# Kernel optimization log

Measured on AMD Instinct MI355X. Metric: run time of the kernel, lower is better.

The kernel has to match this reference:

```python
import jax, jax.numpy as jnp
import numpy as np

B, H, W, C = 8, 64, 64, 256
NUM_GROUPS = 32
EPS = 1e-6  # flax GroupNorm default


def setup_inputs() -> dict:
    key = jax.random.key(0)
    ks = jax.random.split(key, 9)
    x = jax.random.normal(ks[0], (B, H, W, C), dtype=jnp.float32)
    init = lambda k, shape: jax.random.normal(k, shape, dtype=jnp.float32) * 0.02
    return {
        "x": x,
        "gn_scale": jnp.ones((C,), jnp.float32),
        "gn_bias": jnp.zeros((C,), jnp.float32),
        "wq": init(ks[1], (C, C)), "bq": jnp.zeros((C,), jnp.float32),
        "wk": init(ks[2], (C, C)), "bk": jnp.zeros((C,), jnp.float32),
        "wv": init(ks[3], (C, C)), "bv": jnp.zeros((C,), jnp.float32),
        "wo": init(ks[4], (C, C)), "bo": jnp.zeros((C,), jnp.float32),
    }


def group_norm(x, scale, bias, num_groups, eps):
    b, h, w, c = x.shape
    xg = x.reshape(b, h, w, num_groups, c // num_groups)
    mean = jnp.mean(xg, axis=(1, 2, 4), keepdims=True)
    var = jnp.mean(jnp.square(xg - mean), axis=(1, 2, 4), keepdims=True)
    xn = (xg - mean) * jax.lax.rsqrt(var + eps)
    return xn.reshape(b, h, w, c) * scale + bias


def reference(x, gn_scale, gn_bias, wq, bq, wk, bk, wv, bv, wo, bo):
    b, h, w, c = x.shape
    hn = group_norm(x, gn_scale, gn_bias, NUM_GROUPS, EPS)
    hf = hn.reshape(b, h * w, c)  # (B, S, C)
    q = hf @ wq + bq
    k = hf @ wk + bk
    v = hf @ wv + bv
    scaling = jnp.sqrt(jnp.float32(c)).astype(x.dtype)
    attn = jax.nn.softmax(jnp.einsum('bsc,btc->bst', q, k) / scaling, axis=-1)
    out = jnp.einsum('bst,btc->bsc', attn, v)
    out = out @ wo + bo
    return out.reshape(b, h, w, c) + x
```

## Files before the change

kernel.cpp:

```cpp
#include <hip/hip_runtime.h>

#define NB   8
#define SS   4096
#define CC   256
#define NG   32
#define CPG  8
#define EPSV 1e-6f
#define MTOT (NB * SS)

typedef short bf16x8 __attribute__((ext_vector_type(8)));
typedef unsigned short u16x8 __attribute__((ext_vector_type(8)));
typedef float f32x4  __attribute__((ext_vector_type(4)));
typedef float f32x16 __attribute__((ext_vector_type(16)));
typedef int   i32x4  __attribute__((ext_vector_type(4)));
typedef int   i32x8  __attribute__((ext_vector_type(8)));
typedef unsigned char u8;

typedef __attribute__((address_space(1))) const unsigned int as1_u32;
typedef __attribute__((address_space(3))) unsigned int as3_u32;

__device__ __forceinline__ unsigned short f2bf(float f) {
  unsigned int u = __builtin_bit_cast(unsigned int, f);
  u = (u + 0x7FFFu + ((u >> 16) & 1u)) >> 16;
  return (unsigned short)u;
}
__device__ __forceinline__ u8 f2fp8(float f) {
  return (u8)(__builtin_amdgcn_cvt_pk_fp8_f32(f, f, 0, 0) & 0xFF);
}
__device__ __forceinline__ void dma16(const u8* src, u8* lds) {
  __builtin_amdgcn_global_load_lds((as1_u32*)src, (as3_u32*)lds, 16, 0, 0);
}
__device__ __forceinline__ float fast_exp2(float x) {
#if __has_builtin(__builtin_amdgcn_exp2f)
  return __builtin_amdgcn_exp2f(x);
#else
  return exp2f(x);
#endif
}

__global__ __launch_bounds__(256) void gn_stats_part_kernel(
    const float* __restrict__ x, float* __restrict__ part) {
  const int b = blockIdx.x >> 5, slice = blockIdx.x & 31;
  const int tid = threadIdx.x;
  const int g = tid & 31;
  const int p8 = tid >> 5;
  const float* base = x + ((size_t)(b * SS + slice * 128 + p8) * CC + g * CPG);
  float s = 0.f, ss = 0.f;
#pragma unroll
  for (int it = 0; it < 16; it++) {
    const float4* p = (const float4*)(base + (size_t)it * 8 * CC);
    float4 a = p[0], c = p[1];
    s  += (a.x + a.y) + (a.z + a.w) + (c.x + c.y) + (c.z + c.w);
    ss += (a.x*a.x + a.y*a.y) + (a.z*a.z + a.w*a.w)
        + (c.x*c.x + c.y*c.y) + (c.z*c.z + c.w*c.w);
  }
  s  += __shfl_xor(s, 32);
  ss += __shfl_xor(ss, 32);
  __shared__ float lsum[4][32], lssum[4][32];
  const int wv = tid >> 6, lane = tid & 63;
  if (lane < 32) { lsum[wv][lane] = s; lssum[wv][lane] = ss; }
  __syncthreads();
  if (tid < 32) {
    float ts  = (lsum[0][tid] + lsum[1][tid]) + (lsum[2][tid] + lsum[3][tid]);
    float tss = (lssum[0][tid] + lssum[1][tid]) + (lssum[2][tid] + lssum[3][tid]);
    float* dst = part + ((size_t)(b * 32 + tid) * 32 + slice) * 2;
    dst[0] = ts; dst[1] = tss;
  }
}

__global__ __launch_bounds__(256) void prep_wt_kernel(
    const float* __restrict__ w0, const float* __restrict__ w1,
    const float* __restrict__ w2, const float* __restrict__ w3,
    unsigned short* __restrict__ wt,
    const float* __restrict__ part, float* __restrict__ stats) {
  __shared__ float t[64][68];
  if (blockIdx.y == 4) {
    if (blockIdx.x == 0) {
      const int bg = threadIdx.x;
      const float* src = part + (size_t)bg * 64;
      float s = 0.f, ss = 0.f;
#pragma unroll
      for (int sl = 0; sl < 32; sl++) { s += src[sl * 2]; ss += src[sl * 2 + 1]; }
      const float inv = 1.f / (float)(SS * CPG);
      float mean = s * inv;
      float var  = ss * inv - mean * mean;
      stats[bg * 2]     = mean;
      stats[bg * 2 + 1] = rsqrtf(var + EPSV);
    }
    return;
  }
  int which = blockIdx.y;
  const float* W = (which == 0) ? w0 : (which == 1) ? w1 : (which == 2) ? w2 : w3;
  int tx = (blockIdx.x & 3) * 64;
  int ty = (blockIdx.x >> 2) * 64;
  int tid = threadIdx.x;
  int row = tid >> 4;
  int col = (tid & 15) * 4;
#pragma unroll
  for (int i = 0; i < 4; i++) {
    float4 v = *(const float4*)(W + (size_t)(ty + row + i * 16) * CC + tx + col);
    *(float4*)(&t[row + i * 16][col]) = v;
  }
  __syncthreads();
#pragma unroll
  for (int i = 0; i < 4; i++) {
    int n = row + i * 16;
    ushort4 o;
    o.x = f2bf(t[col + 0][n]);
    o.y = f2bf(t[col + 1][n]);
    o.z = f2bf(t[col + 2][n]);
    o.w = f2bf(t[col + 3][n]);
    *(ushort4*)(wt + (size_t)which * CC * CC + (size_t)(tx + n) * CC + ty + col) = o;
  }
}

__global__ __launch_bounds__(256) void gn_norm_kernel(const float* __restrict__ x,
                                                      const float* __restrict__ stats,
                                                      const float* __restrict__ gamma,
                                                      const float* __restrict__ beta,
                                                      unsigned short* __restrict__ hn) {
  int i8 = blockIdx.x * 256 + threadIdx.x;
  int c8 = (i8 & 31) * 8;
  size_t row = (size_t)(i8 >> 5);
  int b = (int)(row >> 12);
  int sidx = (b * NG + (c8 >> 3)) * 2;
  float mean = stats[sidx], rstd = stats[sidx + 1];
  const float4* xp = (const float4*)(x + row * CC + c8);
  float4 v0 = xp[0], v1 = xp[1];
  const float4* gp = (const float4*)(gamma + c8);
  float4 g0 = gp[0], g1 = gp[1];
  const float4* bp = (const float4*)(beta + c8);
  float4 b0 = bp[0], b1 = bp[1];
  u16x8 o;
  o[0] = f2bf((v0.x - mean) * rstd * g0.x + b0.x);
  o[1] = f2bf((v0.y - mean) * rstd * g0.y + b0.y);
  o[2] = f2bf((v0.z - mean) * rstd * g0.z + b0.z);
  o[3] = f2bf((v0.w - mean) * rstd * g0.w + b0.w);
  o[4] = f2bf((v1.x - mean) * rstd * g1.x + b1.x);
  o[5] = f2bf((v1.y - mean) * rstd * g1.y + b1.y);
  o[6] = f2bf((v1.z - mean) * rstd * g1.z + b1.z);
  o[7] = f2bf((v1.w - mean) * rstd * g1.w + b1.w);
  *(u16x8*)(hn + row * CC + c8) = o;
}


__global__ __launch_bounds__(256) void qkv_gemm_kernel(
    const unsigned short* __restrict__ A,
    const unsigned short* __restrict__ WT,
    const float* __restrict__ bq, const float* __restrict__ bk, const float* __restrict__ bv,
    u8* __restrict__ qo, u8* __restrict__ ko, u8* __restrict__ vt) {
  __shared__ __align__(1024) u8 smem[65536];
  u8* As0 = smem;
  u8* As1 = smem + 16384;
  u8* Bs  = smem + 32768;

  const int which = blockIdx.z;
  const u8* Bwb = (const u8*)(WT + (size_t)which * CC * CC);
  const float* bias = (which == 0) ? bq : (which == 1) ? bk : bv;

  const int m0 = blockIdx.x * 256;
  const int n0 = blockIdx.y * 64;
  const int tid = threadIdx.x;
  const int wave = tid >> 6, lane = tid & 63;
  const int l32 = lane & 31, h = lane >> 5;

  const u8* Ab = (const u8*)A;

  const int am = tid >> 2;
  const int aslot = tid & 3;
  const size_t asrc_row = (size_t)(m0 + am) * 512;
  const int asrc_ch = ((aslot ^ (am & 3)) << 4);
  const int bn = tid >> 5;
  const int bslot = tid & 31;

#pragma unroll
  for (int i = 0; i < 8; i++) {
    int n = i * 8 + bn;
    dma16(Bwb + (size_t)(n0 + n) * 512 + ((bslot ^ (n & 31)) << 4),
          Bs + i * 4096 + tid * 16);
  }
#pragma unroll
  for (int i = 0; i < 4; i++)
    dma16(Ab + asrc_row + (size_t)i * 64 * 512 + asrc_ch, As0 + i * 4096 + tid * 16);
  __syncthreads();

  f32x16 acc[2][2] = {};
  const int arow0 = (wave * 64 + l32) * 64;
  const int nrow0 = l32 * 512;
  const int aswz = l32 & 3;
  const int bswz = l32;

#pragma unroll
  for (int s = 0; s < 8; ++s) {
    u8* cur = (s & 1) ? As1 : As0;
    if (s < 7) {
      u8* nxt = (s & 1) ? As0 : As1;
      size_t koff = (size_t)(s + 1) * 64;
#pragma unroll
      for (int i = 0; i < 4; i++)
        dma16(Ab + asrc_row + (size_t)i * 64 * 512 + koff + asrc_ch,
              nxt + i * 4096 + tid * 16);
    }
#pragma unroll
    for (int ks = 0; ks < 2; ks++) {
      bf16x8 af0 = *(const bf16x8*)(cur + arow0 + (((h + 2 * ks) ^ aswz) << 4));
      bf16x8 af1 = *(const bf16x8*)(cur + arow0 + 32 * 64 + (((h + 2 * ks) ^ aswz) << 4));
      bf16x8 bf0 = *(const bf16x8*)(Bs + nrow0 + (((s * 4 + h + 2 * ks) ^ bswz) << 4));
      bf16x8 bf1 = *(const bf16x8*)(Bs + nrow0 + 32 * 512 + (((s * 4 + h + 2 * ks) ^ bswz) << 4));
      acc[0][0] = __builtin_amdgcn_mfma_f32_32x32x16_bf16(af0, bf0, acc[0][0], 0, 0, 0);
      acc[0][1] = __builtin_amdgcn_mfma_f32_32x32x16_bf16(af0, bf1, acc[0][1], 0, 0, 0);
      acc[1][0] = __builtin_amdgcn_mfma_f32_32x32x16_bf16(af1, bf0, acc[1][0], 0, 0, 0);
      acc[1][1] = __builtin_amdgcn_mfma_f32_32x32x16_bf16(af1, bf1, acc[1][1], 0, 0, 0);
    }
    __syncthreads();
  }

  if (which < 2) {
    u8* out = (which == 0) ? qo : ko;
#pragma unroll
    for (int nt = 0; nt < 2; nt++) {
      int n = n0 + nt * 32 + l32;
      float bv_ = bias[n];
#pragma unroll
      for (int mt = 0; mt < 2; mt++)
#pragma unroll
        for (int r = 0; r < 16; r++) {
          int m = m0 + wave * 64 + mt * 32 + (r & 3) + 8 * (r >> 2) + 4 * h;
          out[(size_t)m * CC + n] = f2fp8(acc[mt][nt][r] + bv_);
        }
    }
  } else {
    int bb = m0 >> 12;
#pragma unroll
    for (int nt = 0; nt < 2; nt++) {
      int n = n0 + nt * 32 + l32;
      float bv_ = bias[n];
#pragma unroll
      for (int mt = 0; mt < 2; mt++)
#pragma unroll
        for (int g = 0; g < 4; g++) {
          int mg = m0 + wave * 64 + mt * 32 + g * 8 + 4 * h;
          int w = __builtin_amdgcn_cvt_pk_fp8_f32(acc[mt][nt][g*4+0] + bv_, acc[mt][nt][g*4+1] + bv_, 0, 0);
          w = __builtin_amdgcn_cvt_pk_fp8_f32(acc[mt][nt][g*4+2] + bv_, acc[mt][nt][g*4+3] + bv_, w, 1);
          *(unsigned int*)(vt + (size_t)bb * CC * SS + (size_t)n * SS + (mg & 4095)) = (unsigned int)w;
        }
    }
  }
}

__global__ __launch_bounds__(256) void out_gemm_kernel(
    const unsigned short* __restrict__ A,
    const unsigned short* __restrict__ WT,
    const float* __restrict__ bias,
    const float* __restrict__ residual,
    float* __restrict__ Of) {
  __shared__ __align__(1024) u8 smem[65536];
  u8* As0 = smem;
  u8* As1 = smem + 16384;
  u8* Bs  = smem + 32768;

  const u8* Bwb = (const u8*)(WT + (size_t)3 * CC * CC);
  const int m0 = blockIdx.x * 256;
  const int n0 = blockIdx.y * 64;
  const int tid = threadIdx.x;
  const int wave = tid >> 6, lane = tid & 63;
  const int l32 = lane & 31, h = lane >> 5;

  const u8* Ab = (const u8*)A;
  const int am = tid >> 2;
  const int aslot = tid & 3;
  const size_t asrc_row = (size_t)(m0 + am) * 512;
  const int asrc_ch = ((aslot ^ (am & 3)) << 4);
  const int bn = tid >> 5;
  const int bslot = tid & 31;

#pragma unroll
  for (int i = 0; i < 8; i++) {
    int n = i * 8 + bn;
    dma16(Bwb + (size_t)(n0 + n) * 512 + ((bslot ^ (n & 31)) << 4),
          Bs + i * 4096 + tid * 16);
  }
#pragma unroll
  for (int i = 0; i < 4; i++)
    dma16(Ab + asrc_row + (size_t)i * 64 * 512 + asrc_ch, As0 + i * 4096 + tid * 16);
  __syncthreads();

  f32x16 acc[2][2] = {};
  const int arow0 = (wave * 64 + l32) * 64;
  const int nrow0 = l32 * 512;
  const int aswz = l32 & 3;
  const int bswz = l32;

#pragma unroll
  for (int s = 0; s < 8; ++s) {
    u8* cur = (s & 1) ? As1 : As0;
    if (s < 7) {
      u8* nxt = (s & 1) ? As0 : As1;
      size_t koff = (size_t)(s + 1) * 64;
#pragma unroll
      for (int i = 0; i < 4; i++)
        dma16(Ab + asrc_row + (size_t)i * 64 * 512 + koff + asrc_ch,
              nxt + i * 4096 + tid * 16);
    }
#pragma unroll
    for (int ks = 0; ks < 2; ks++) {
      bf16x8 af0 = *(const bf16x8*)(cur + arow0 + (((h + 2 * ks) ^ aswz) << 4));
      bf16x8 af1 = *(const bf16x8*)(cur + arow0 + 32 * 64 + (((h + 2 * ks) ^ aswz) << 4));
      bf16x8 bf0 = *(const bf16x8*)(Bs + nrow0 + (((s * 4 + h + 2 * ks) ^ bswz) << 4));
      bf16x8 bf1 = *(const bf16x8*)(Bs + nrow0 + 32 * 512 + (((s * 4 + h + 2 * ks) ^ bswz) << 4));
      acc[0][0] = __builtin_amdgcn_mfma_f32_32x32x16_bf16(af0, bf0, acc[0][0], 0, 0, 0);
      acc[0][1] = __builtin_amdgcn_mfma_f32_32x32x16_bf16(af0, bf1, acc[0][1], 0, 0, 0);
      acc[1][0] = __builtin_amdgcn_mfma_f32_32x32x16_bf16(af1, bf0, acc[1][0], 0, 0, 0);
      acc[1][1] = __builtin_amdgcn_mfma_f32_32x32x16_bf16(af1, bf1, acc[1][1], 0, 0, 0);
    }
    __syncthreads();
  }

#pragma unroll
  for (int nt = 0; nt < 2; nt++) {
    int n = n0 + nt * 32 + l32;
    float bv_ = bias[n];
#pragma unroll
    for (int mt = 0; mt < 2; mt++)
#pragma unroll
      for (int r = 0; r < 16; r++) {
        int m = m0 + wave * 64 + mt * 32 + (r & 3) + 8 * (r >> 2) + 4 * h;
        Of[(size_t)m * CC + n] = acc[mt][nt][r] + bv_ + residual[(size_t)m * CC + n];
      }
  }
}

#define BR 64

__global__ __launch_bounds__(256, 2) void flash_attn_kernel(
    const u8* __restrict__ Qg,
    const u8* __restrict__ Kg,
    const u8* __restrict__ Vtg,
    unsigned short* __restrict__ Og) {
  __shared__ __align__(1024) u8 smem[65536 + 512];
  u8* KA  = smem;
  u8* KBb = smem + 16384;
  u8* VB  = smem + 32768;

  const int bid = blockIdx.x;
  const int b = bid & 7, q0 = (bid >> 3) * BR;
  const int tid = threadIdx.x;
  const int wave = tid >> 6, lane = tid & 63;
  const int l32 = lane & 31, h = lane >> 5;
  const int wm = wave >> 1, wn = wave & 1;

  const u8* Qb  = Qg  + (size_t)b * SS * CC;
  const u8* Kb  = Kg  + (size_t)b * SS * CC;
  const u8* Vtb = Vtg + (size_t)b * CC * SS;

  const int kkey = tid >> 4, kc16 = tid & 15;
  const u8* ksrc0 = Kb + (size_t)kkey * CC + ((kc16 ^ (kkey & 15)) << 4);
  const int vch = tid >> 3;
  const int vs  = (tid & 7) ^ (vch & 7);
  const u8* vsrc0 = Vtb + (size_t)vch * SS + (vs << 4);

  i32x8 qf[4];
  {
    const u8* qrow = Qb + (size_t)(q0 + wm * 32 + l32) * CC + h * 32;
#pragma unroll
    for (int t = 0; t < 4; t++) qf[t] = *(const i32x8*)(qrow + t * 64);
  }

  f32x16 oacc[8] = {};
  float ll = 0.f;

#pragma unroll
  for (int i = 0; i < 4; i++)
    dma16(ksrc0 + (size_t)i * 16 * CC, KA + i * 4096 + tid * 16);

  const int kswz = l32 & 15;
  const int vswz = l32 & 7;

  for (int jp = 0; jp < 32; ++jp) {
    int w0[4], w1[4], o0[4];

    __syncthreads();
    {
      size_t krow = (size_t)jp * 128 + 64;
#pragma unroll
      for (int i = 0; i < 4; i++)
        dma16(ksrc0 + (krow + (size_t)i * 16) * CC, KBb + i * 4096 + tid * 16);
      size_t vbase = (size_t)jp * 128;
#pragma unroll
      for (int i = 0; i < 8; i++)
        dma16(vsrc0 + (size_t)i * 32 * SS + vbase, VB + i * 4096 + tid * 16);
    }
    {
      f32x16 sacc = {};
      const u8* kb = KA + (wn * 32 + l32) * 256;
      __builtin_amdgcn_s_setprio(1);
#pragma unroll
      for (int t = 0; t < 4; t++) {
        i32x4 r0 = *(const i32x4*)(kb + (((t * 4 + 2 * h)     ^ kswz) << 4));
        i32x4 r1 = *(const i32x4*)(kb + (((t * 4 + 2 * h + 1) ^ kswz) << 4));
        i32x8 kf = __builtin_shufflevector(r0, r1, 0, 1, 2, 3, 4, 5, 6, 7);
        sacc = __builtin_amdgcn_mfma_scale_f32_32x32x64_f8f6f4(
            kf, qf[t], sacc, 0, 0, 0, 0x7F7F7F7F, 0, 0x7F7F7F7F);
      }
      __builtin_amdgcn_s_setprio(0);
#pragma unroll
      for (int g = 0; g < 4; g++) {
        float p0 = fast_exp2(fminf(sacc[g * 4 + 0] * 0.09016844f, 7.213475f));
        float p1 = fast_exp2(fminf(sacc[g * 4 + 1] * 0.09016844f, 7.213475f));
        float p2 = fast_exp2(fminf(sacc[g * 4 + 2] * 0.09016844f, 7.213475f));
        float p3 = fast_exp2(fminf(sacc[g * 4 + 3] * 0.09016844f, 7.213475f));
        ll += (p0 + p1) + (p2 + p3);
        int wv_ = __builtin_amdgcn_cvt_pk_fp8_f32(p0, p1, 0, 0);
        w0[g] = __builtin_amdgcn_cvt_pk_fp8_f32(p2, p3, wv_, 1);
      }
#pragma unroll
      for (int g = 0; g < 4; g++) o0[g] = __shfl_xor(w0[g], 32);
    }

    __syncthreads();
    if (jp + 1 < 32) {
      size_t krow = (size_t)(jp + 1) * 128;
#pragma unroll
      for (int i = 0; i < 4; i++)
        dma16(ksrc0 + (krow + (size_t)i * 16) * CC, KA + i * 4096 + tid * 16);
    }
    {
      f32x16 sacc = {};
      const u8* kb = KBb + (wn * 32 + l32) * 256;
      __builtin_amdgcn_s_setprio(1);
#pragma unroll
      for (int t = 0; t < 4; t++) {
        i32x4 r0 = *(const i32x4*)(kb + (((t * 4 + 2 * h)     ^ kswz) << 4));
        i32x4 r1 = *(const i32x4*)(kb + (((t * 4 + 2 * h + 1) ^ kswz) << 4));
        i32x8 kf = __builtin_shufflevector(r0, r1, 0, 1, 2, 3, 4, 5, 6, 7);
        sacc = __builtin_amdgcn_mfma_scale_f32_32x32x64_f8f6f4(
            kf, qf[t], sacc, 0, 0, 0, 0x7F7F7F7F, 0, 0x7F7F7F7F);
      }
      __builtin_amdgcn_s_setprio(0);
#pragma unroll
      for (int g = 0; g < 4; g++) {
        float p0 = fast_exp2(fminf(sacc[g * 4 + 0] * 0.09016844f, 7.213475f));
        float p1 = fast_exp2(fminf(sacc[g * 4 + 1] * 0.09016844f, 7.213475f));
        float p2 = fast_exp2(fminf(sacc[g * 4 + 2] * 0.09016844f, 7.213475f));
        float p3 = fast_exp2(fminf(sacc[g * 4 + 3] * 0.09016844f, 7.213475f));
        ll += (p0 + p1) + (p2 + p3);
        int wv_ = __builtin_amdgcn_cvt_pk_fp8_f32(p0, p1, 0, 0);
        w1[g] = __builtin_amdgcn_cvt_pk_fp8_f32(p2, p3, wv_, 1);
      }
    }

    int pa_[8];
#pragma unroll
    for (int g = 0; g < 4; g++) {
      int o1 = __shfl_xor(w1[g], 32);
      pa_[2 * g]     = (h == 0) ? w0[g] : o1;
      pa_[2 * g + 1] = (h == 0) ? o0[g] : w1[g];
    }
    i32x8 pa = {pa_[0], pa_[1], pa_[2], pa_[3], pa_[4], pa_[5], pa_[6], pa_[7]};

    __builtin_amdgcn_s_setprio(1);
#pragma unroll
    for (int nt = 0; nt < 8; nt++) {
      const u8* vb = VB + (nt * 32 + l32) * 128;
      i32x4 r0 = *(const i32x4*)(vb + (((4 * h + 2 * wn)     ^ vswz) << 4));
      i32x4 r1 = *(const i32x4*)(vb + (((4 * h + 2 * wn + 1) ^ vswz) << 4));
      i32x8 vf = __builtin_shufflevector(r0, r1, 0, 1, 2, 3, 4, 5, 6, 7);
      oacc[nt] = __builtin_amdgcn_mfma_scale_f32_32x32x64_f8f6f4(
          pa, vf, oacc[nt], 0, 0, 0, 0x7F7F7F7F, 0, 0x7F7F7F7F);
    }
    __builtin_amdgcn_s_setprio(0);
  }

  __syncthreads();
  ll += __shfl_xor(ll, 32);
  float* Lred = (float*)(smem + 65536);
  if (h == 0) Lred[wn * 64 + wm * 32 + l32] = ll;

  float* scratch = (float*)smem;
  {
    float* z = scratch + (size_t)(wm * 2 + (1 - wn)) * 4096;
#pragma unroll
    for (int ntg = 0; ntg < 8; ntg++) {
      if ((ntg >> 2) != wn) {
        int nt = ntg & 3;
#pragma unroll
        for (int r = 0; r < 16; r++) {
          int row = (r & 3) + 8 * (r >> 2) + 4 * h;
          z[row * 128 + nt * 32 + l32] = oacc[ntg][r];
        }
      }
    }
  }
  __syncthreads();
  {
    const float* z = scratch + (size_t)(wm * 2 + wn) * 4096;
#pragma unroll
    for (int ntg = 0; ntg < 8; ntg++) {
      if ((ntg >> 2) == wn) {
        int nt = ntg & 3;
#pragma unroll
        for (int r = 0; r < 16; r++) {
          int row = (r & 3) + 8 * (r >> 2) + 4 * h;
          float inv = 1.f / (Lred[wm * 32 + row] + Lred[64 + wm * 32 + row]);
          float v = oacc[ntg][r] + z[row * 128 + nt * 32 + l32];
          Og[((size_t)b * SS + q0 + wm * 32 + row) * CC + wn * 128 + nt * 32 + l32]
              = f2bf(v * inv);
        }
      }
    }
  }
}

extern "C" void kernel_launch(void* const* d_in, const int* in_sizes, int n_in,
                              void* d_out, int out_size, void* d_ws, size_t ws_size,
                              hipStream_t stream) {
  const float* x   = (const float*)d_in[0];
  const float* gsc = (const float*)d_in[1];
  const float* gbi = (const float*)d_in[2];
  const float* wq  = (const float*)d_in[3];
  const float* bq  = (const float*)d_in[4];
  const float* wk  = (const float*)d_in[5];
  const float* bk  = (const float*)d_in[6];
  const float* wv  = (const float*)d_in[7];
  const float* bv  = (const float*)d_in[8];
  const float* wo  = (const float*)d_in[9];
  const float* bo  = (const float*)d_in[10];
  float* out = (float*)d_out;

  char* ws = (char*)d_ws;
  const size_t MAT = (size_t)MTOT * CC;
  float* stats        = (float*)ws;
  unsigned short* wt  = (unsigned short*)(ws + 4096);
  unsigned short* hn  = wt + (size_t)4 * CC * CC;
  unsigned short* ao  = hn + MAT;
  u8* q  = (u8*)(ao + MAT);
  u8* k  = q + MAT;
  u8* vt = k + MAT;

  float* part = (float*)ao;

  gn_stats_part_kernel<<<NB * NG, 256, 0, stream>>>(x, part);
  prep_wt_kernel<<<dim3(16, 5), 256, 0, stream>>>(wq, wk, wv, wo, wt, part, stats);
  gn_norm_kernel<<<(int)(MAT / 8 / 256), 256, 0, stream>>>(x, stats, gsc, gbi, hn);

  qkv_gemm_kernel<<<dim3(MTOT / 256, CC / 64, 3), 256, 0, stream>>>(
      hn, wt, bq, bk, bv, q, k, vt);

  flash_attn_kernel<<<NB * (SS / BR), 256, 0, stream>>>(q, k, vt, ao);

  out_gemm_kernel<<<dim3(MTOT / 256, CC / 64), 256, 0, stream>>>(ao, wt, bo, x, out);
}
```

Baseline: 244.4 us.

## Split PV output columns across waves via LDS-shared P tile for higher occupancy

Restructures the flash attention loop to process 64 keys per iteration, with each wave pair splitting the 256 output columns instead of splitting keys. P fragments are exchanged through a small swizzled LDS buffer rather than cross-lane shuffles. This halves the output accumulators and removes the final cross-wave reduction through LDS, allowing 3 blocks per CU with a smaller shared memory footprint. The trade-off is twice as many loop iterations and barriers, plus extra LDS traffic for the P tile.

```diff
diff --git a/kernel.cpp b/kernel.cpp
--- a/kernel.cpp
+++ b/kernel.cpp
@@ -332,22 +332,24 @@
 
 #define BR 64
 
-__global__ __launch_bounds__(256, 2) void flash_attn_kernel(
+__global__ __launch_bounds__(256, 3) void flash_attn_kernel(
     const u8* __restrict__ Qg,
     const u8* __restrict__ Kg,
     const u8* __restrict__ Vtg,
     unsigned short* __restrict__ Og) {
-  __shared__ __align__(1024) u8 smem[65536 + 512];
-  u8* KA  = smem;
-  u8* KBb = smem + 16384;
+  __shared__ __align__(1024) u8 smem[53760];
+  u8* KB0 = smem;
+  u8* KB1 = smem + 16384;
   u8* VB  = smem + 32768;
+  u8* Ps  = smem + 49152;
+  float* Lred = (float*)(smem + 53248);
 
   const int bid = blockIdx.x;
   const int b = bid & 7, q0 = (bid >> 3) * BR;
   const int tid = threadIdx.x;
   const int wave = tid >> 6, lane = tid & 63;
   const int l32 = lane & 31, h = lane >> 5;
-  const int wm = wave >> 1, wn = wave & 1;
+  const int wm = wave >> 1, wc = wave & 1;
 
   const u8* Qb  = Qg  + (size_t)b * SS * CC;
   const u8* Kb  = Kg  + (size_t)b * SS * CC;
@@ -355,8 +357,8 @@
 
   const int kkey = tid >> 4, kc16 = tid & 15;
   const u8* ksrc0 = Kb + (size_t)kkey * CC + ((kc16 ^ (kkey & 15)) << 4);
-  const int vch = tid >> 3;
-  const int vs  = (tid & 7) ^ (vch & 7);
+  const int vch = tid >> 2;
+  const int vs  = (tid & 3) ^ (vch & 3);
   const u8* vsrc0 = Vtb + (size_t)vch * SS + (vs << 4);
 
   i32x8 qf[4];
@@ -366,33 +368,32 @@
     for (int t = 0; t < 4; t++) qf[t] = *(const i32x8*)(qrow + t * 64);
   }
 
-  f32x16 oacc[8] = {};
+  f32x16 oacc[4] = {};
   float ll = 0.f;
 
 #pragma unroll
   for (int i = 0; i < 4; i++)
-    dma16(ksrc0 + (size_t)i * 16 * CC, KA + i * 4096 + tid * 16);
+    dma16(ksrc0 + (size_t)i * 16 * CC, KB0 + i * 4096 + tid * 16);
 
   const int kswz = l32 & 15;
-  const int vswz = l32 & 7;
-
-  for (int jp = 0; jp < 32; ++jp) {
-    int w0[4], w1[4], o0[4];
+  const int vswz = l32 & 3;
+  const int pswz = l32 & 7;
+
+  for (int j = 0; j < SS / BR; ++j) {
+    const u8* Kcur = (j & 1) ? KB1 : KB0;
+    u8* Knxt = (j & 1) ? KB0 : KB1;
 
     __syncthreads();
     {
-      size_t krow = (size_t)jp * 128 + 64;
+      size_t vbase = (size_t)j * 64;
 #pragma unroll
       for (int i = 0; i < 4; i++)
-        dma16(ksrc0 + (krow + (size_t)i * 16) * CC, KBb + i * 4096 + tid * 16);
-      size_t vbase = (size_t)jp * 128;
-#pragma unroll
-      for (int i = 0; i < 8; i++)
-        dma16(vsrc0 + (size_t)i * 32 * SS + vbase, VB + i * 4096 + tid * 16);
-    }
+        dma16(vsrc0 + (size_t)i * 64 * SS + vbase, VB + i * 4096 + tid * 16);
+    }
+
     {
       f32x16 sacc = {};
-      const u8* kb = KA + (wn * 32 + l32) * 256;
+      const u8* kb = Kcur + (wc * 32 + l32) * 256;
       __builtin_amdgcn_s_setprio(1);
 #pragma unroll
       for (int t = 0; t < 4; t++) {
@@ -403,6 +404,7 @@
             kf, qf[t], sacc, 0, 0, 0, 0x7F7F7F7F, 0, 0x7F7F7F7F);
       }
       __builtin_amdgcn_s_setprio(0);
+      u8* pb = Ps + (wm * 32 + l32) * 64;
 #pragma unroll
       for (int g = 0; g < 4; g++) {
         float p0 = fast_exp2(fminf(sacc[g * 4 + 0] * 0.09016844f, 7.213475f));
@@ -411,103 +413,57 @@
         float p3 = fast_exp2(fminf(sacc[g * 4 + 3] * 0.09016844f, 7.213475f));
         ll += (p0 + p1) + (p2 + p3);
         int wv_ = __builtin_amdgcn_cvt_pk_fp8_f32(p0, p1, 0, 0);
-        w0[g] = __builtin_amdgcn_cvt_pk_fp8_f32(p2, p3, wv_, 1);
+        wv_ = __builtin_amdgcn_cvt_pk_fp8_f32(p2, p3, wv_, 1);
+        *(unsigned int*)(pb + (((wc * 4 + g) ^ pswz) << 3) + 4 * h) = (unsigned int)wv_;
       }
-#pragma unroll
-      for (int g = 0; g < 4; g++) o0[g] = __shfl_xor(w0[g], 32);
     }
 
     __syncthreads();
-    if (jp + 1 < 32) {
-      size_t krow = (size_t)(jp + 1) * 128;
+    if (j + 1 < SS / BR) {
+      size_t krow = (size_t)(j + 1) * 64;
 #pragma unroll
       for (int i = 0; i < 4; i++)
-        dma16(ksrc0 + (krow + (size_t)i * 16) * CC, KA + i * 4096 + tid * 16);
-    }
+        dma16(ksrc0 + (krow + (size_t)i * 16) * CC, Knxt + i * 4096 + tid * 16);
+    }
+
     {
-      f32x16 sacc = {};
-      const u8* kb = KBb + (wn * 32 + l32) * 256;
+      unsigned long pf[4];
+      const u8* pb = Ps + (wm * 32 + l32) * 64;
+#pragma unroll
+      for (int ki = 0; ki < 4; ki++)
+        pf[ki] = *(const unsigned long*)(pb + (((4 * h + ki) ^ pswz) << 3));
+      i32x8 pa;
+#pragma unroll
+      for (int ki = 0; ki < 4; ki++) {
+        pa[2 * ki]     = (int)(unsigned int)pf[ki];
+        pa[2 * ki + 1] = (int)(unsigned int)(pf[ki] >> 32);
+      }
       __builtin_amdgcn_s_setprio(1);
 #pragma unroll
-      for (int t = 0; t < 4; t++) {
-        i32x4 r0 = *(const i32x4*)(kb + (((t * 4 + 2 * h)     ^ kswz) << 4));
-        i32x4 r1 = *(const i32x4*)(kb + (((t * 4 + 2 * h + 1) ^ kswz) << 4));
-        i32x8 kf = __builtin_shufflevector(r0, r1, 0, 1, 2, 3, 4, 5, 6, 7);
-        sacc = __builtin_amdgcn_mfma_scale_f32_32x32x64_f8f6f4(
-            kf, qf[t], sacc, 0, 0, 0, 0x7F7F7F7F, 0, 0x7F7F7F7F);
+      for (int nt = 0; nt < 4; nt++) {
+        const u8* vb = VB + (wc * 128 + nt * 32 + l32) * 64;
+        i32x4 r0 = *(const i32x4*)(vb + (((2 * h)     ^ vswz) << 4));
+        i32x4 r1 = *(const i32x4*)(vb + (((2 * h + 1) ^ vswz) << 4));
+        i32x8 vf = __builtin_shufflevector(r0, r1, 0, 1, 2, 3, 4, 5, 6, 7);
+        oacc[nt] = __builtin_amdgcn_mfma_scale_f32_32x32x64_f8f6f4(
+            pa, vf, oacc[nt], 0, 0, 0, 0x7F7F7F7F, 0, 0x7F7F7F7F);
       }
       __builtin_amdgcn_s_setprio(0);
-#pragma unroll
-      for (int g = 0; g < 4; g++) {
-        float p0 = fast_exp2(fminf(sacc[g * 4 + 0] * 0.09016844f, 7.213475f));
-        float p1 = fast_exp2(fminf(sacc[g * 4 + 1] * 0.09016844f, 7.213475f));
-        float p2 = fast_exp2(fminf(sacc[g * 4 + 2] * 0.09016844f, 7.213475f));
-        float p3 = fast_exp2(fminf(sacc[g * 4 + 3] * 0.09016844f, 7.213475f));
-        ll += (p0 + p1) + (p2 + p3);
-        int wv_ = __builtin_amdgcn_cvt_pk_fp8_f32(p0, p1, 0, 0);
-        w1[g] = __builtin_amdgcn_cvt_pk_fp8_f32(p2, p3, wv_, 1);
-      }
-    }
-
-    int pa_[8];
-#pragma unroll
-    for (int g = 0; g < 4; g++) {
-      int o1 = __shfl_xor(w1[g], 32);
-      pa_[2 * g]     = (h == 0) ? w0[g] : o1;
-      pa_[2 * g + 1] = (h == 0) ? o0[g] : w1[g];
-    }
-    i32x8 pa = {pa_[0], pa_[1], pa_[2], pa_[3], pa_[4], pa_[5], pa_[6], pa_[7]};
-
-    __builtin_amdgcn_s_setprio(1);
-#pragma unroll
-    for (int nt = 0; nt < 8; nt++) {
-      const u8* vb = VB + (nt * 32 + l32) * 128;
-      i32x4 r0 = *(const i32x4*)(vb + (((4 * h + 2 * wn)     ^ vswz) << 4));
-      i32x4 r1 = *(const i32x4*)(vb + (((4 * h + 2 * wn + 1) ^ vswz) << 4));
-      i32x8 vf = __builtin_shufflevector(r0, r1, 0, 1, 2, 3, 4, 5, 6, 7);
-      oacc[nt] = __builtin_amdgcn_mfma_scale_f32_32x32x64_f8f6f4(
-          pa, vf, oacc[nt], 0, 0, 0, 0x7F7F7F7F, 0, 0x7F7F7F7F);
-    }
-    __builtin_amdgcn_s_setprio(0);
-  }
-
+    }
+  }
+
+  ll += __shfl_xor(ll, 32);
+  if (h == 0) Lred[wc * 64 + wm * 32 + l32] = ll;
   __syncthreads();
-  ll += __shfl_xor(ll, 32);
-  float* Lred = (float*)(smem + 65536);
-  if (h == 0) Lred[wn * 64 + wm * 32 + l32] = ll;
-
-  float* scratch = (float*)smem;
-  {
-    float* z = scratch + (size_t)(wm * 2 + (1 - wn)) * 4096;
-#pragma unroll
-    for (int ntg = 0; ntg < 8; ntg++) {
-      if ((ntg >> 2) != wn) {
-        int nt = ntg & 3;
-#pragma unroll
-        for (int r = 0; r < 16; r++) {
-          int row = (r & 3) + 8 * (r >> 2) + 4 * h;
-          z[row * 128 + nt * 32 + l32] = oacc[ntg][r];
-        }
-      }
-    }
-  }
-  __syncthreads();
-  {
-    const float* z = scratch + (size_t)(wm * 2 + wn) * 4096;
-#pragma unroll
-    for (int ntg = 0; ntg < 8; ntg++) {
-      if ((ntg >> 2) == wn) {
-        int nt = ntg & 3;
-#pragma unroll
-        for (int r = 0; r < 16; r++) {
-          int row = (r & 3) + 8 * (r >> 2) + 4 * h;
-          float inv = 1.f / (Lred[wm * 32 + row] + Lred[64 + wm * 32 + row]);
-          float v = oacc[ntg][r] + z[row * 128 + nt * 32 + l32];
-          Og[((size_t)b * SS + q0 + wm * 32 + row) * CC + wn * 128 + nt * 32 + l32]
-              = f2bf(v * inv);
-        }
-      }
-    }
+
+#pragma unroll
+  for (int r = 0; r < 16; r++) {
+    int row = (r & 3) + 8 * (r >> 2) + 4 * h;
+    float inv = 1.f / (Lred[wm * 32 + row] + Lred[64 + wm * 32 + row]);
+    size_t base = ((size_t)b * SS + q0 + wm * 32 + row) * CC + wc * 128 + l32;
+#pragma unroll
+    for (int nt = 0; nt < 4; nt++)
+      Og[base + nt * 32] = f2bf(oacc[nt][r] * inv);
   }
 }
 
```

Measured after the change: 245.8 us. Within noise of the previous version (+0.5%).

## Triple-buffer A tiles in QKV and output GEMMs with partial vmcnt barriers

Applied to the files above, without the earlier changes.

Both projection GEMM kernels move from double to triple buffering of the A operand in LDS, prefetching two k-steps ahead. Full syncthreads are replaced by explicit vmcnt waits that leave the newest DMA batch in flight before each barrier. The goal is to hide global-to-LDS load latency behind MFMA work. The cost is LDS per block growing from 64KB to 80KB, which can lower occupancy, and the hand-counted vmcnt values must match the outstanding loads exactly.

```diff
diff --git a/kernel.cpp b/kernel.cpp
--- a/kernel.cpp
+++ b/kernel.cpp
@@ -37,6 +37,13 @@
   return exp2f(x);
 #endif
 }
+
+#define CV_BARRIER(N)                                              \
+  do {                                                             \
+    asm volatile("s_waitcnt vmcnt(" #N ")" ::: "memory");          \
+    __builtin_amdgcn_s_barrier();                                  \
+    __builtin_amdgcn_sched_barrier(0);                             \
+  } while (0)
 
 __global__ __launch_bounds__(256) void gn_stats_part_kernel(
     const float* __restrict__ x, float* __restrict__ part) {
@@ -149,10 +156,11 @@
     const unsigned short* __restrict__ WT,
     const float* __restrict__ bq, const float* __restrict__ bk, const float* __restrict__ bv,
     u8* __restrict__ qo, u8* __restrict__ ko, u8* __restrict__ vt) {
-  __shared__ __align__(1024) u8 smem[65536];
-  u8* As0 = smem;
-  u8* As1 = smem + 16384;
-  u8* Bs  = smem + 32768;
+  __shared__ __align__(1024) u8 smem[81920];
+  u8* A0 = smem;
+  u8* A1 = smem + 16384;
+  u8* A2 = smem + 32768;
+  u8* Bs = smem + 49152;
 
   const int which = blockIdx.z;
   const u8* Bwb = (const u8*)(WT + (size_t)which * CC * CC);
@@ -181,8 +189,11 @@
   }
 #pragma unroll
   for (int i = 0; i < 4; i++)
-    dma16(Ab + asrc_row + (size_t)i * 64 * 512 + asrc_ch, As0 + i * 4096 + tid * 16);
-  __syncthreads();
+    dma16(Ab + asrc_row + (size_t)i * 64 * 512 + asrc_ch, A0 + i * 4096 + tid * 16);
+#pragma unroll
+  for (int i = 0; i < 4; i++)
+    dma16(Ab + asrc_row + (size_t)i * 64 * 512 + 64 + asrc_ch, A1 + i * 4096 + tid * 16);
+  CV_BARRIER(4);
 
   f32x16 acc[2][2] = {};
   const int arow0 = (wave * 64 + l32) * 64;
@@ -192,10 +203,11 @@
 
 #pragma unroll
   for (int s = 0; s < 8; ++s) {
-    u8* cur = (s & 1) ? As1 : As0;
-    if (s < 7) {
-      u8* nxt = (s & 1) ? As0 : As1;
-      size_t koff = (size_t)(s + 1) * 64;
+    u8* const bufs[3] = {A0, A1, A2};
+    u8* cur = bufs[s % 3];
+    if (s + 2 < 8) {
+      u8* nxt = bufs[(s + 2) % 3];
+      size_t koff = (size_t)(s + 2) * 64;
 #pragma unroll
       for (int i = 0; i < 4; i++)
         dma16(Ab + asrc_row + (size_t)i * 64 * 512 + koff + asrc_ch,
@@ -212,7 +224,8 @@
       acc[1][0] = __builtin_amdgcn_mfma_f32_32x32x16_bf16(af1, bf0, acc[1][0], 0, 0, 0);
       acc[1][1] = __builtin_amdgcn_mfma_f32_32x32x16_bf16(af1, bf1, acc[1][1], 0, 0, 0);
     }
-    __syncthreads();
+    if (s < 6)      CV_BARRIER(4);
+    else if (s < 7) CV_BARRIER(0);
   }
 
   if (which < 2) {
@@ -254,10 +267,11 @@
     const float* __restrict__ bias,
     const float* __restrict__ residual,
     float* __restrict__ Of) {
-  __shared__ __align__(1024) u8 smem[65536];
-  u8* As0 = smem;
-  u8* As1 = smem + 16384;
-  u8* Bs  = smem + 32768;
+  __shared__ __align__(1024) u8 smem[81920];
+  u8* A0 = smem;
+  u8* A1 = smem + 16384;
+  u8* A2 = smem + 32768;
+  u8* Bs = smem + 49152;
 
   const u8* Bwb = (const u8*)(WT + (size_t)3 * CC * CC);
   const int m0 = blockIdx.x * 256;
@@ -282,8 +296,11 @@
   }
 #pragma unroll
   for (int i = 0; i < 4; i++)
-    dma16(Ab + asrc_row + (size_t)i * 64 * 512 + asrc_ch, As0 + i * 4096 + tid * 16);
-  __syncthreads();
+    dma16(Ab + asrc_row + (size_t)i * 64 * 512 + asrc_ch, A0 + i * 4096 + tid * 16);
+#pragma unroll
+  for (int i = 0; i < 4; i++)
+    dma16(Ab + asrc_row + (size_t)i * 64 * 512 + 64 + asrc_ch, A1 + i * 4096 + tid * 16);
+  CV_BARRIER(4);
 
   f32x16 acc[2][2] = {};
   const int arow0 = (wave * 64 + l32) * 64;
@@ -293,10 +310,11 @@
 
 #pragma unroll
   for (int s = 0; s < 8; ++s) {
-    u8* cur = (s & 1) ? As1 : As0;
-    if (s < 7) {
-      u8* nxt = (s & 1) ? As0 : As1;
-      size_t koff = (size_t)(s + 1) * 64;
+    u8* const bufs[3] = {A0, A1, A2};
+    u8* cur = bufs[s % 3];
+    if (s + 2 < 8) {
+      u8* nxt = bufs[(s + 2) % 3];
+      size_t koff = (size_t)(s + 2) * 64;
 #pragma unroll
       for (int i = 0; i < 4; i++)
         dma16(Ab + asrc_row + (size_t)i * 64 * 512 + koff + asrc_ch,
@@ -313,7 +331,8 @@
       acc[1][0] = __builtin_amdgcn_mfma_f32_32x32x16_bf16(af1, bf0, acc[1][0], 0, 0, 0);
       acc[1][1] = __builtin_amdgcn_mfma_f32_32x32x16_bf16(af1, bf1, acc[1][1], 0, 0, 0);
     }
-    __syncthreads();
+    if (s < 6)      CV_BARRIER(4);
+    else if (s < 7) CV_BARRIER(0);
   }
 
 #pragma unroll
```

New measurement: 240.0 us (median of 2 runs). No clear change (-1.8%).
